# Performance work log

Hardware: AMD Instinct MI355X
Metric: run time of the kernel (lower is better)

The kernel has to match this reference:

```python
import jax, jax.numpy as jnp
import numpy as np

H = W = 256
SIZE, STRIDE = 16, 8
NUMS = (H - SIZE) // STRIDE + 1   # 31
L = NUMS * NUMS                   # 961
S2 = SIZE * SIZE                  # 256
EPS = 1e-5
B, C = 2, 64


def _rel_pos_index(h, w):
    ch, cw = np.arange(h), np.arange(w)
    coords = np.stack(np.meshgrid(ch, cw, indexing='ij'))      # [2,h,w]
    cf = coords.reshape(2, -1)                                  # [2,h*w]
    rel = (cf[:, :, None] - cf[:, None, :]).transpose(1, 2, 0)  # [L,L,2]
    rel = rel.copy()
    rel[:, :, 0] += h - 1
    rel[:, :, 1] += w - 1
    rel[:, :, 0] *= 2 * w - 1
    return jnp.asarray(rel.sum(-1))                             # [L,L] int

REL_IDX = _rel_pos_index(NUMS, NUMS)


def unfold(x):
    # torch.nn.Unfold(kernel=SIZE, stride=STRIDE): [B,C,H,W] -> [B, C*S2, L]
    b, c = x.shape[:2]
    p = jax.lax.conv_general_dilated_patches(x, (SIZE, SIZE), (STRIDE, STRIDE), 'VALID')
    return p.reshape(b, c * S2, L)


def fold(cols, c):
    # torch.nn.Fold: [B, c*S2, L] -> [B, c, H, W] via overlap scatter-add
    b = cols.shape[0]
    p = cols.reshape(b, c, SIZE, SIZE, NUMS, NUMS)          # [b,c,kh,kw,oh,ow]
    idx = jnp.arange(SIZE)[:, None] + STRIDE * jnp.arange(NUMS)[None, :]  # [SIZE,NUMS]
    hfull = idx[:, None, :, None]   # [kh,1,oh,1]
    wfull = idx[None, :, None, :]   # [1,kw,1,ow]
    out = jnp.zeros((b, c, H, W), cols.dtype)
    return out.at[:, :, hfull, wfull].add(p)


def fg_mean_std(region, mask):
    # masked spatial mean / std; region = x*mask already
    s = region.sum((2, 3))                                   # [B,C]
    num = mask.sum((2, 3))                                   # [B,1]
    mu = (s / (num + EPS))[:, :, None, None]                 # [B,C,1,1]
    # region + (1-mask)*mu - mu == region - mask*mu
    var = (((region - mask * mu) ** 2).sum((2, 3)) / (num + EPS))[:, :, None, None]
    return mu, jnp.sqrt(var + EPS)


def setup_inputs() -> dict:
    key = jax.random.key(0)
    ks = jax.random.split(key, 12)
    x = jax.random.normal(ks[0], (B, C, H, W), jnp.float32)
    mask = (jax.random.uniform(ks[1], (B, 1, H, W)) > 0.5).astype(jnp.float32)
    def v(k, scale=0.02, off=0.0):
        return off + scale * jax.random.normal(k, (C,), jnp.float32)
    return {
        'x': x, 'mask': mask,
        'fg_gamma': v(ks[2]), 'fg_beta': v(ks[3]),
        'bg_gamma': v(ks[4]), 'bg_beta': v(ks[5]),
        'q_gamma': v(ks[6], off=1.0), 'q_beta': v(ks[7]),
        'k_gamma': v(ks[8], off=1.0), 'k_beta': v(ks[9]),
        'bias_table': 0.02 * jax.random.normal(ks[10], ((2 * NUMS - 1) ** 2,), jnp.float32),
    }


def reference(x, mask, fg_gamma, fg_beta, bg_gamma, bg_beta,
              q_gamma, q_beta, k_gamma, k_beta, bias_table):
    om = 1.0 - mask
    mean_b, std_b = fg_mean_std(x * om, om)
    normalized = (x - mean_b) / std_b * om
    norm_bg = (x * (1 + bg_gamma[None, :, None, None]) + bg_beta[None, :, None, None]) * om
    mean_f, std_f = fg_mean_std(x * mask, mask)
    norm_fg = (x - mean_f) / std_f * mask

    # unfold to [B,C,L,S2] (torch: view(B,C,S2,L).permute(0,1,3,2))
    pb = unfold(x * om).reshape(B, C, S2, L).transpose(0, 1, 3, 2)
    npf = unfold(norm_fg).reshape(B, C, S2, L).transpose(0, 1, 3, 2)
    npb = unfold(normalized).reshape(B, C, S2, L).transpose(0, 1, 3, 2)
    pm = unfold(mask).reshape(B, 1, S2, L).transpose(0, 1, 3, 2)
    count_cols = unfold(jnp.ones((1, 1, H, W), x.dtype))     # [1,S2,L]

    # per-patch masked stats (note: 'std' is actually variance, as in original)
    num = (1.0 - pm).sum(3)                                   # [B,1,L]
    mu1 = pb.sum(3) / (num + EPS)                             # [B,C,L]
    var1 = (((pb - (1.0 - pm) * mu1[..., None]) ** 2).sum(3)) / (num + EPS)
    mu4 = npb.sum(3) / (num + EPS)
    numm = pm.sum(3)
    mu3 = npf.sum(3) / (numm + EPS)

    q = mu3 * q_gamma[None, :, None] + q_beta[None, :, None]
    k = mu4 * k_gamma[None, :, None] + k_beta[None, :, None]

    bias = bias_table[REL_IDX.reshape(-1)].reshape(L, L)
    Smat = jax.nn.softmax(jnp.einsum('bcl,bcm->blm', q, k) + bias[None], axis=-1)
    patch_back = jnp.einsum('blm,bcm->bcl', Smat, mu1)[..., None]   # [B,C,L,1]
    patch_std = jnp.einsum('blm,bcm->bcl', Smat, var1)[..., None]

    npf2 = npf * patch_std + patch_back                        # [B,C,L,S2]
    cols = npf2.transpose(0, 1, 3, 2).reshape(B, C * S2, L)
    cnt = fold(count_cols, 1)                                  # [1,1,H,W]
    nf = fold(cols, C) / cnt
    nf = (nf * (1 + fg_gamma[None, :, None, None]) + fg_beta[None, :, None, None]) * mask
    return nf + norm_bg
```

## Files before the change

### kernel.cpp

```cpp
#include <hip/hip_runtime.h>
#include <hip/hip_fp16.h>
#include <cmath>

constexpr int H = 256, W = 256;
constexpr int NUMS = 31;
constexpr int L = NUMS * NUMS;
constexpr int B = 2, C = 64;
constexpr float EPS = 1e-5f;

constexpr int NL = 8;
constexpr int NGROUP = 121;
constexpr int LPAD = 968;
constexpr int MPAD = 976;
constexpr int M2 = 488;

typedef __fp16 h2 __attribute__((ext_vector_type(2)));

__device__ inline h2 pk2(float a, float b) {
#if __has_builtin(__builtin_amdgcn_cvt_pkrtz)
    return __builtin_amdgcn_cvt_pkrtz(a, b);
#else
    h2 r; r.x = (__fp16)a; r.y = (__fp16)b; return r;
#endif
}
__device__ inline float h2f(h2 v) { return __builtin_bit_cast(float, v); }
__device__ inline h2 f2h(float v) { return __builtin_bit_cast(h2, v); }

#if __has_builtin(__builtin_amdgcn_fdot2)
#define FDOT2(a, b, c) __builtin_amdgcn_fdot2((a), (b), (c), false)
#else
#define FDOT2(a, b, c) ((c) + (float)(a).x * (float)(b).x + (float)(a).y * (float)(b).y)
#endif

__global__ __launch_bounds__(256) void cellsum_kernel(
    const float* __restrict__ x, const float* __restrict__ mask,
    float4* __restrict__ cellsA, float* __restrict__ cellsM)
{
    int cr = blockIdx.x, c = blockIdx.y, b = blockIdx.z;
    int t = threadIdx.x, r = t >> 5, cc = t & 31;
    const float* xp = x + (((size_t)(b * C + c) * H) + cr * 8 + r) * W + cc * 8;
    const float* mp = mask + (((size_t)b * H) + cr * 8 + r) * W + cc * 8;

    float s0 = 0.f, s1 = 0.f, s2 = 0.f, s3 = 0.f, nf = 0.f;
#pragma unroll
    for (int q = 0; q < 2; ++q) {
        float4 xv = ((const float4*)xp)[q];
        float4 mv = ((const float4*)mp)[q];
        float xs[4] = {xv.x, xv.y, xv.z, xv.w};
        float ms[4] = {mv.x, mv.y, mv.z, mv.w};
#pragma unroll
        for (int j = 0; j < 4; ++j) {
            float xx = xs[j], m = ms[j], om = 1.f - m;
            s0 += xx * om; s1 += xx * xx * om;
            s2 += xx;      s3 += xx * xx;
            nf += m;
        }
    }
    s0 += __shfl_xor(s0, 32); s1 += __shfl_xor(s1, 32);
    s2 += __shfl_xor(s2, 32); s3 += __shfl_xor(s3, 32);
    nf += __shfl_xor(nf, 32);

    __shared__ float red[4][32][5];
    int wv = t >> 6;
    if ((t & 63) < 32) {
        red[wv][cc][0] = s0; red[wv][cc][1] = s1; red[wv][cc][2] = s2;
        red[wv][cc][3] = s3; red[wv][cc][4] = nf;
    }
    __syncthreads();
    if (t < 32) {
        float a0 = red[0][t][0] + red[1][t][0] + red[2][t][0] + red[3][t][0];
        float a1 = red[0][t][1] + red[1][t][1] + red[2][t][1] + red[3][t][1];
        float a2 = red[0][t][2] + red[1][t][2] + red[2][t][2] + red[3][t][2];
        float a3 = red[0][t][3] + red[1][t][3] + red[2][t][3] + red[3][t][3];
        float an = red[0][t][4] + red[1][t][4] + red[2][t][4] + red[3][t][4];
        int cell = cr * 32 + t;
        cellsA[((size_t)b * 1024 + cell) * C + c] = make_float4(a0, a1, a2, a3);
        if (c == 0) cellsM[(size_t)b * 1024 + cell] = an;
    }
}

__global__ __launch_bounds__(256) void stats_kernel(
    const float4* __restrict__ cellsA, const float* __restrict__ cellsM,
    float* __restrict__ stats)
{
    int c = blockIdx.x, b = blockIdx.y, t = threadIdx.x;
    float s0 = 0.f, s1 = 0.f, s2 = 0.f, s3 = 0.f, nf = 0.f;
    for (int e = t; e < 1024; e += 256) {
        float4 v = cellsA[((size_t)b * 1024 + e) * C + c];
        s0 += v.x; s1 += v.y; s2 += v.z; s3 += v.w;
        nf += cellsM[(size_t)b * 1024 + e];
    }
#pragma unroll
    for (int off = 32; off; off >>= 1) {
        s0 += __shfl_xor(s0, off); s1 += __shfl_xor(s1, off);
        s2 += __shfl_xor(s2, off); s3 += __shfl_xor(s3, off);
        nf += __shfl_xor(nf, off);
    }
    __shared__ float red[4][5];
    if ((t & 63) == 0) {
        red[t >> 6][0] = s0; red[t >> 6][1] = s1; red[t >> 6][2] = s2;
        red[t >> 6][3] = s3; red[t >> 6][4] = nf;
    }
    __syncthreads();
    if (t == 0) {
        float a0 = red[0][0] + red[1][0] + red[2][0] + red[3][0];
        float a1 = red[0][1] + red[1][1] + red[2][1] + red[3][1];
        float a2 = red[0][2] + red[1][2] + red[2][2] + red[3][2];
        float a3 = red[0][3] + red[1][3] + red[2][3] + red[3][3];
        float an = red[0][4] + red[1][4] + red[2][4] + red[3][4];
        float numbg = (float)(H * W) - an;
        float mu_b = a0 / (numbg + EPS);
        float var_b = (a1 - 2.f * mu_b * a0 + mu_b * mu_b * numbg) / (numbg + EPS);
        float sxfg = a2 - a0, sxxfg = a3 - a1;
        float mu_f = sxfg / (an + EPS);
        float var_f = (sxxfg - 2.f * mu_f * sxfg + mu_f * mu_f * an) / (an + EPS);
        float* st = stats + ((size_t)b * C + c) * 4;
        st[0] = mu_b; st[1] = 1.f / sqrtf(var_b + EPS);
        st[2] = mu_f; st[3] = 1.f / sqrtf(var_f + EPS);
    }
}

__global__ __launch_bounds__(256) void patchfinal_kernel(
    const float4* __restrict__ cellsA, const float* __restrict__ cellsM,
    const float* __restrict__ stats,
    const float* __restrict__ qg, const float* __restrict__ qb,
    const float* __restrict__ kg, const float* __restrict__ kb,
    float* __restrict__ qTT, float* __restrict__ kTT, float2* __restrict__ mvh)
{
    int lq = blockIdx.x, b = blockIdx.y;
    int t = threadIdx.x, ls = t >> 6, c = t & 63;
    int l = lq * 4 + ls;

    float mu1 = 0.f, var1 = 0.f, qv = 0.f, kv = 0.f;
    if (l < L) {
        int lh = l / 31, lw = l % 31;
        int e00 = lh * 32 + lw;
        size_t base = (size_t)b * 1024;
        float4 s00 = cellsA[(base + e00) * C + c];
        float4 s01 = cellsA[(base + e00 + 1) * C + c];
        float4 s10 = cellsA[(base + e00 + 32) * C + c];
        float4 s11 = cellsA[(base + e00 + 33) * C + c];
        float sxbg = s00.x + s01.x + s10.x + s11.x;
        float sxxbg = s00.y + s01.y + s10.y + s11.y;
        float sxall = s00.z + s01.z + s10.z + s11.z;
        float nfg = cellsM[base + e00] + cellsM[base + e00 + 1]
                  + cellsM[base + e00 + 32] + cellsM[base + e00 + 33];
        float numbg = 256.f - nfg;
        float rb = 1.f / (numbg + EPS), rf = 1.f / (nfg + EPS);
        const float* st = stats + ((size_t)b * C + c) * 4;
        float mu_b = st[0], isb = st[1], mu_f = st[2], isf = st[3];
        mu1 = sxbg * rb;
        var1 = (sxxbg - 2.f * mu1 * sxbg + mu1 * mu1 * numbg) * rb;
        float mu4 = (sxbg - mu_b * numbg) * isb * rb;
        float sxfg = sxall - sxbg;
        float mu3 = (sxfg - mu_f * nfg) * isf * rf;
        qv = mu3 * qg[c] + qb[c];
        kv = mu4 * kg[c] + kb[c];
    }
    qTT[((size_t)(b * C + c)) * LPAD + l] = qv;
    kTT[((size_t)(b * C + c)) * MPAD + l] = kv;

    __shared__ float smu[4][64], svar[4][64];
    smu[ls][c] = mu1; svar[ls][c] = var1;
    __syncthreads();
    if (t < 128) {
        int p = t >> 6, cc = t & 63;
        h2 mp_ = pk2(smu[2 * p][cc], smu[2 * p + 1][cc]);
        h2 vp_ = pk2(svar[2 * p][cc], svar[2 * p + 1][cc]);
        mvh[((size_t)b * M2 + lq * 2 + p) * C + cc] = make_float2(h2f(mp_), h2f(vp_));
    }
}

__global__ __launch_bounds__(512) void attn_kernel(
    const float* __restrict__ qTT, const float* __restrict__ kTT,
    const float2* __restrict__ mvh, const float* __restrict__ bias_table,
    float* __restrict__ pbTc, float* __restrict__ psTc)
{
    __shared__ float4 wlds[M2][2];
    __shared__ float parts[8][NL][65][2];
    __shared__ float rsp[8][NL];

    int g = blockIdx.x, b = blockIdx.y;
    int t = threadIdx.x, l0 = g * NL;
    int m0 = t, m1 = t + 512;
    int m1c = m1 < MPAD ? m1 : MPAD - 1;

    int lhs[NL], lws[NL];
#pragma unroll
    for (int li = 0; li < NL; ++li) {
        int l = l0 + li; if (l > L - 1) l = L - 1;
        lhs[li] = l / 31; lws[li] = l % 31;
    }

    float dot0[NL] = {0, 0, 0, 0, 0, 0, 0, 0};
    float dot1[NL] = {0, 0, 0, 0, 0, 0, 0, 0};
    const float* kbase = kTT + (size_t)b * C * MPAD;
    const float* qbase = qTT + (size_t)b * C * LPAD + l0;
#pragma unroll 4
    for (int c = 0; c < C; ++c) {
        float k0 = kbase[(size_t)c * MPAD + m0];
        float k1 = kbase[(size_t)c * MPAD + m1c];
        const float* qp = qbase + (size_t)c * LPAD;
#pragma unroll
        for (int li = 0; li < NL; ++li) {
            float q = qp[li];
            dot0[li] = fmaf(q, k0, dot0[li]);
            dot1[li] = fmaf(q, k1, dot1[li]);
        }
    }

    float e0[NL], e1[NL];
    float psum[NL] = {0, 0, 0, 0, 0, 0, 0, 0};
    {
        int mh = m0 / 31, mw = m0 - mh * 31;
#pragma unroll
        for (int li = 0; li < NL; ++li) {
            float bias = bias_table[(lhs[li] - mh + 30) * 61 + (lws[li] - mw + 30)];
            e0[li] = __expf(dot0[li] + bias);
            psum[li] += e0[li];
        }
    }
    if (m1 < L) {
        int mh = m1 / 31, mw = m1 - mh * 31;
#pragma unroll
        for (int li = 0; li < NL; ++li) {
            float bias = bias_table[(lhs[li] - mh + 30) * 61 + (lws[li] - mw + 30)];
            e1[li] = __expf(dot1[li] + bias);
            psum[li] += e1[li];
        }
    } else {
#pragma unroll
        for (int li = 0; li < NL; ++li) e1[li] = 0.f;
    }

    {
        float n0[NL], n1[NL];
#pragma unroll
        for (int li = 0; li < NL; ++li) {
            n0[li] = __shfl_down(e0[li], 1);
            n1[li] = __shfl_down(e1[li], 1);
        }
        if (!(t & 1)) {
            wlds[m0 >> 1][0] = make_float4(h2f(pk2(e0[0], n0[0])), h2f(pk2(e0[1], n0[1])),
                                           h2f(pk2(e0[2], n0[2])), h2f(pk2(e0[3], n0[3])));
            wlds[m0 >> 1][1] = make_float4(h2f(pk2(e0[4], n0[4])), h2f(pk2(e0[5], n0[5])),
                                           h2f(pk2(e0[6], n0[6])), h2f(pk2(e0[7], n0[7])));
            if (m1 < MPAD) {
                wlds[m1 >> 1][0] = make_float4(h2f(pk2(e1[0], n1[0])), h2f(pk2(e1[1], n1[1])),
                                               h2f(pk2(e1[2], n1[2])), h2f(pk2(e1[3], n1[3])));
                wlds[m1 >> 1][1] = make_float4(h2f(pk2(e1[4], n1[4])), h2f(pk2(e1[5], n1[5])),
                                               h2f(pk2(e1[6], n1[6])), h2f(pk2(e1[7], n1[7])));
            }
        }
    }
#pragma unroll
    for (int li = 0; li < NL; ++li) {
        float v = psum[li];
#pragma unroll
        for (int off = 32; off; off >>= 1) v += __shfl_xor(v, off);
        if ((t & 63) == 0) rsp[t >> 6][li] = v;
    }
    __syncthreads();

    int wv = t >> 6, c = t & 63;
    float accb[NL] = {0, 0, 0, 0, 0, 0, 0, 0};
    float accs[NL] = {0, 0, 0, 0, 0, 0, 0, 0};
    const float2* vbase = mvh + (size_t)b * M2 * C + c;
    int mstart = wv * 61;
#pragma unroll 2
    for (int i = 0; i < 61; ++i) {
        int m2 = mstart + i;
        float4 wa = wlds[m2][0];
        float4 wb = wlds[m2][1];
        float2 v = vbase[(size_t)m2 * C];
        h2 vb = f2h(v.x), vs = f2h(v.y);
        accb[0] = FDOT2(f2h(wa.x), vb, accb[0]); accs[0] = FDOT2(f2h(wa.x), vs, accs[0]);
        accb[1] = FDOT2(f2h(wa.y), vb, accb[1]); accs[1] = FDOT2(f2h(wa.y), vs, accs[1]);
        accb[2] = FDOT2(f2h(wa.z), vb, accb[2]); accs[2] = FDOT2(f2h(wa.z), vs, accs[2]);
        accb[3] = FDOT2(f2h(wa.w), vb, accb[3]); accs[3] = FDOT2(f2h(wa.w), vs, accs[3]);
        accb[4] = FDOT2(f2h(wb.x), vb, accb[4]); accs[4] = FDOT2(f2h(wb.x), vs, accs[4]);
        accb[5] = FDOT2(f2h(wb.y), vb, accb[5]); accs[5] = FDOT2(f2h(wb.y), vs, accs[5]);
        accb[6] = FDOT2(f2h(wb.z), vb, accb[6]); accs[6] = FDOT2(f2h(wb.z), vs, accs[6]);
        accb[7] = FDOT2(f2h(wb.w), vb, accb[7]); accs[7] = FDOT2(f2h(wb.w), vs, accs[7]);
    }
#pragma unroll
    for (int li = 0; li < NL; ++li) {
        parts[wv][li][c][0] = accb[li];
        parts[wv][li][c][1] = accs[li];
    }
    __syncthreads();

    {
        int li = t & 7, co = t >> 3;
        float sb = 0.f, ss = 0.f, rs = 0.f;
#pragma unroll
        for (int w = 0; w < 8; ++w) {
            sb += parts[w][li][co][0];
            ss += parts[w][li][co][1];
            rs += rsp[w][li];
        }
        if (l0 + li < L) {
            float inv = 1.f / rs;
            size_t o = ((size_t)(b * C + co)) * LPAD + l0 + li;
            pbTc[o] = sb * inv;
            psTc[o] = ss * inv;
        }
    }
}

__global__ __launch_bounds__(256) void out_kernel(
    const float* __restrict__ x, const float* __restrict__ mask,
    const float* __restrict__ stats,
    const float* __restrict__ pbTc, const float* __restrict__ psTc,
    const float* __restrict__ fgg, const float* __restrict__ fgb,
    const float* __restrict__ bgg, const float* __restrict__ bgb,
    float* __restrict__ out)
{
    int idx = blockIdx.x * 256 + threadIdx.x;
    int w4 = idx & (W / 4 - 1);
    int rest = idx >> 6;
    int h = rest & (H - 1);
    int bc = rest >> 8;
    int c = bc & (C - 1);
    int b = bc >> 6;
    int w = w4 * 4;

    size_t pix = ((size_t)bc * H + h) * W + w;
    float4 xv = *(const float4*)&x[pix];
    float4 mv = *(const float4*)&mask[((size_t)b * H + h) * W + w];

    const float* st = stats + (size_t)bc * 4;
    float mu_f = st[2], isf = st[3];

    int hq = h >> 3, wq = w >> 3;
    int ph0 = hq > 0 ? hq - 1 : 0;
    int ph1 = hq < NUMS ? hq : NUMS - 1;
    int pw0 = wq > 0 ? wq - 1 : 0;
    int pw1 = wq < NUMS ? wq : NUMS - 1;

    const float* pbc = pbTc + (size_t)bc * LPAD;
    const float* psc = psTc + (size_t)bc * LPAD;

    float sstd = 0.f, sback = 0.f;
    for (int ph = ph0; ph <= ph1; ++ph) {
        int base = ph * 31;
        for (int pw = pw0; pw <= pw1; ++pw) {
            sstd += psc[base + pw];
            sback += pbc[base + pw];
        }
    }
    float rcnt = 1.f / (float)((ph1 - ph0 + 1) * (pw1 - pw0 + 1));
    float ga = 1.f + fgg[c], be = fgb[c];
    float gb_ = 1.f + bgg[c], bb = bgb[c];

    float xs[4] = {xv.x, xv.y, xv.z, xv.w};
    float ms_[4] = {mv.x, mv.y, mv.z, mv.w};
    float4 res;
    float* rp = &res.x;
#pragma unroll
    for (int j = 0; j < 4; ++j) {
        float nfg_px = (xs[j] - mu_f) * isf * ms_[j];
        float nf = (nfg_px * sstd + sback) * rcnt;
        rp[j] = (nf * ga + be) * ms_[j] + (xs[j] * gb_ + bb) * (1.f - ms_[j]);
    }
    *(float4*)&out[pix] = res;
}

extern "C" void kernel_launch(void* const* d_in, const int* in_sizes, int n_in,
                              void* d_out, int out_size, void* d_ws, size_t ws_size,
                              hipStream_t stream)
{
    const float* x    = (const float*)d_in[0];
    const float* mask = (const float*)d_in[1];
    const float* fgg  = (const float*)d_in[2];
    const float* fgb  = (const float*)d_in[3];
    const float* bgg  = (const float*)d_in[4];
    const float* bgb  = (const float*)d_in[5];
    const float* qg   = (const float*)d_in[6];
    const float* qb   = (const float*)d_in[7];
    const float* kg   = (const float*)d_in[8];
    const float* kb   = (const float*)d_in[9];
    const float* bt   = (const float*)d_in[10];
    float* out = (float*)d_out;

    float* ws = (float*)d_ws;
    float4* cellsA = (float4*)ws;
    float* cellsM  = ws + (size_t)B * 1024 * C * 4;
    float* stats   = cellsM + (size_t)B * 1024;
    float* qTT     = stats + (size_t)B * C * 4;
    float* kTT     = qTT + (size_t)B * C * LPAD;
    float2* mvh    = (float2*)(kTT + (size_t)B * C * MPAD);
    float* pbTc    = (float*)mvh + (size_t)B * M2 * C * 2;
    float* psTc    = pbTc + (size_t)B * C * LPAD;

    cellsum_kernel<<<dim3(32, C, B), 256, 0, stream>>>(x, mask, cellsA, cellsM);
    stats_kernel<<<dim3(C, B), 256, 0, stream>>>(cellsA, cellsM, stats);
    patchfinal_kernel<<<dim3(241, B), 256, 0, stream>>>(
        cellsA, cellsM, stats, qg, qb, kg, kb, qTT, kTT, mvh);
    attn_kernel<<<dim3(NGROUP, B), 512, 0, stream>>>(qTT, kTT, mvh, bt, pbTc, psTc);
    out_kernel<<<(B * C * H * W / 4 + 255) / 256, 256, 0, stream>>>(
        x, mask, stats, pbTc, psTc, fgg, fgb, bgg, bgb, out);
}
```

Before: 69.32 us.

## Halve attention rows per block and precompute fold averages in a separate kernel

```diff
diff --git a/kernel.cpp b/kernel.cpp
--- a/kernel.cpp
+++ b/kernel.cpp
@@ -8,8 +8,8 @@
 constexpr int B = 2, C = 64;
 constexpr float EPS = 1e-5f;
 
-constexpr int NL = 8;
-constexpr int NGROUP = 121;
+constexpr int NL = 4;
+constexpr int NGROUP = 241;
 constexpr int LPAD = 968;
 constexpr int MPAD = 976;
 constexpr int M2 = 488;
@@ -171,19 +171,17 @@
     }
 }
 
-__global__ __launch_bounds__(512) void attn_kernel(
+__global__ __launch_bounds__(256) void attn_kernel(
     const float* __restrict__ qTT, const float* __restrict__ kTT,
     const float2* __restrict__ mvh, const float* __restrict__ bias_table,
     float* __restrict__ pbTc, float* __restrict__ psTc)
 {
-    __shared__ float4 wlds[M2][2];
-    __shared__ float parts[8][NL][65][2];
-    __shared__ float rsp[8][NL];
+    __shared__ float4 wlds[M2];
+    __shared__ float parts[4][NL][65][2];
+    __shared__ float rsp[4][NL];
 
     int g = blockIdx.x, b = blockIdx.y;
     int t = threadIdx.x, l0 = g * NL;
-    int m0 = t, m1 = t + 512;
-    int m1c = m1 < MPAD ? m1 : MPAD - 1;
 
     int lhs[NL], lws[NL];
 #pragma unroll
@@ -192,65 +190,62 @@
         lhs[li] = l / 31; lws[li] = l % 31;
     }
 
-    float dot0[NL] = {0, 0, 0, 0, 0, 0, 0, 0};
-    float dot1[NL] = {0, 0, 0, 0, 0, 0, 0, 0};
+    int mm[4] = {t, t + 256, t + 512, t + 768};
+    int m3c = mm[3] < MPAD ? mm[3] : MPAD - 1;
+
+    float dot[4][NL];
+#pragma unroll
+    for (int j = 0; j < 4; ++j)
+#pragma unroll
+        for (int li = 0; li < NL; ++li) dot[j][li] = 0.f;
+
     const float* kbase = kTT + (size_t)b * C * MPAD;
     const float* qbase = qTT + (size_t)b * C * LPAD + l0;
-#pragma unroll 4
+#pragma unroll 2
     for (int c = 0; c < C; ++c) {
-        float k0 = kbase[(size_t)c * MPAD + m0];
-        float k1 = kbase[(size_t)c * MPAD + m1c];
+        float k0 = kbase[(size_t)c * MPAD + mm[0]];
+        float k1 = kbase[(size_t)c * MPAD + mm[1]];
+        float k2 = kbase[(size_t)c * MPAD + mm[2]];
+        float k3 = kbase[(size_t)c * MPAD + m3c];
         const float* qp = qbase + (size_t)c * LPAD;
 #pragma unroll
         for (int li = 0; li < NL; ++li) {
             float q = qp[li];
-            dot0[li] = fmaf(q, k0, dot0[li]);
-            dot1[li] = fmaf(q, k1, dot1[li]);
-        }
-    }
-
-    float e0[NL], e1[NL];
-    float psum[NL] = {0, 0, 0, 0, 0, 0, 0, 0};
-    {
-        int mh = m0 / 31, mw = m0 - mh * 31;
-#pragma unroll
-        for (int li = 0; li < NL; ++li) {
-            float bias = bias_table[(lhs[li] - mh + 30) * 61 + (lws[li] - mw + 30)];
-            e0[li] = __expf(dot0[li] + bias);
-            psum[li] += e0[li];
-        }
-    }
-    if (m1 < L) {
-        int mh = m1 / 31, mw = m1 - mh * 31;
-#pragma unroll
-        for (int li = 0; li < NL; ++li) {
-            float bias = bias_table[(lhs[li] - mh + 30) * 61 + (lws[li] - mw + 30)];
-            e1[li] = __expf(dot1[li] + bias);
-            psum[li] += e1[li];
-        }
-    } else {
-#pragma unroll
-        for (int li = 0; li < NL; ++li) e1[li] = 0.f;
-    }
-
-    {
-        float n0[NL], n1[NL];
-#pragma unroll
-        for (int li = 0; li < NL; ++li) {
-            n0[li] = __shfl_down(e0[li], 1);
-            n1[li] = __shfl_down(e1[li], 1);
-        }
-        if (!(t & 1)) {
-            wlds[m0 >> 1][0] = make_float4(h2f(pk2(e0[0], n0[0])), h2f(pk2(e0[1], n0[1])),
-                                           h2f(pk2(e0[2], n0[2])), h2f(pk2(e0[3], n0[3])));
-            wlds[m0 >> 1][1] = make_float4(h2f(pk2(e0[4], n0[4])), h2f(pk2(e0[5], n0[5])),
-                                           h2f(pk2(e0[6], n0[6])), h2f(pk2(e0[7], n0[7])));
-            if (m1 < MPAD) {
-                wlds[m1 >> 1][0] = make_float4(h2f(pk2(e1[0], n1[0])), h2f(pk2(e1[1], n1[1])),
-                                               h2f(pk2(e1[2], n1[2])), h2f(pk2(e1[3], n1[3])));
-                wlds[m1 >> 1][1] = make_float4(h2f(pk2(e1[4], n1[4])), h2f(pk2(e1[5], n1[5])),
-                                               h2f(pk2(e1[6], n1[6])), h2f(pk2(e1[7], n1[7])));
+            dot[0][li] = fmaf(q, k0, dot[0][li]);
+            dot[1][li] = fmaf(q, k1, dot[1][li]);
+            dot[2][li] = fmaf(q, k2, dot[2][li]);
+            dot[3][li] = fmaf(q, k3, dot[3][li]);
+        }
+    }
+
+    float e[4][NL];
+    float psum[NL] = {0.f, 0.f, 0.f, 0.f};
+#pragma unroll
+    for (int j = 0; j < 4; ++j) {
+        int m = mm[j];
+        if (m < L) {
+            int mh = m / 31, mw = m - (m / 31) * 31;
+#pragma unroll
+            for (int li = 0; li < NL; ++li) {
+                float bias = bias_table[(lhs[li] - mh + 30) * 61 + (lws[li] - mw + 30)];
+                e[j][li] = __expf(dot[j][li] + bias);
+                psum[li] += e[j][li];
             }
+        } else {
+#pragma unroll
+            for (int li = 0; li < NL; ++li) e[j][li] = 0.f;
+        }
+    }
+
+#pragma unroll
+    for (int j = 0; j < 4; ++j) {
+        float n0 = __shfl_down(e[j][0], 1);
+        float n1 = __shfl_down(e[j][1], 1);
+        float n2 = __shfl_down(e[j][2], 1);
+        float n3 = __shfl_down(e[j][3], 1);
+        if (!(t & 1) && mm[j] < MPAD) {
+            wlds[mm[j] >> 1] = make_float4(h2f(pk2(e[j][0], n0)), h2f(pk2(e[j][1], n1)),
+                                           h2f(pk2(e[j][2], n2)), h2f(pk2(e[j][3], n3)));
         }
     }
 #pragma unroll
@@ -262,39 +257,55 @@
     }
     __syncthreads();
 
-    int wv = t >> 6, c = t & 63;
-    float accb[NL] = {0, 0, 0, 0, 0, 0, 0, 0};
-    float accs[NL] = {0, 0, 0, 0, 0, 0, 0, 0};
-    const float2* vbase = mvh + (size_t)b * M2 * C + c;
-    int mstart = wv * 61;
-#pragma unroll 2
-    for (int i = 0; i < 61; ++i) {
-        int m2 = mstart + i;
-        float4 wa = wlds[m2][0];
-        float4 wb = wlds[m2][1];
-        float2 v = vbase[(size_t)m2 * C];
-        h2 vb = f2h(v.x), vs = f2h(v.y);
-        accb[0] = FDOT2(f2h(wa.x), vb, accb[0]); accs[0] = FDOT2(f2h(wa.x), vs, accs[0]);
-        accb[1] = FDOT2(f2h(wa.y), vb, accb[1]); accs[1] = FDOT2(f2h(wa.y), vs, accs[1]);
-        accb[2] = FDOT2(f2h(wa.z), vb, accb[2]); accs[2] = FDOT2(f2h(wa.z), vs, accs[2]);
-        accb[3] = FDOT2(f2h(wa.w), vb, accb[3]); accs[3] = FDOT2(f2h(wa.w), vs, accs[3]);
-        accb[4] = FDOT2(f2h(wb.x), vb, accb[4]); accs[4] = FDOT2(f2h(wb.x), vs, accs[4]);
-        accb[5] = FDOT2(f2h(wb.y), vb, accb[5]); accs[5] = FDOT2(f2h(wb.y), vs, accs[5]);
-        accb[6] = FDOT2(f2h(wb.z), vb, accb[6]); accs[6] = FDOT2(f2h(wb.z), vs, accs[6]);
-        accb[7] = FDOT2(f2h(wb.w), vb, accb[7]); accs[7] = FDOT2(f2h(wb.w), vs, accs[7]);
-    }
+    int wv = t >> 6, lane = t & 63;
+    int mg = lane >> 4, ci = lane & 15;
+    float accb[NL][4], accs[NL][4];
+#pragma unroll
+    for (int li = 0; li < NL; ++li)
+#pragma unroll
+        for (int cs = 0; cs < 4; ++cs) { accb[li][cs] = 0.f; accs[li][cs] = 0.f; }
+
+    const float2* vbase = mvh + (size_t)b * M2 * C;
+    int moff = (wv << 2) + mg;
+    for (int i = 0; i < 31; ++i) {
+        int m2 = i * 16 + moff;
+        if (m2 < M2) {
+            float4 w4 = wlds[m2];
+            h2 w0 = f2h(w4.x), w1 = f2h(w4.y), w2 = f2h(w4.z), w3 = f2h(w4.w);
+            const float2* vp = vbase + (size_t)m2 * C + ci;
+#pragma unroll
+            for (int cs = 0; cs < 4; ++cs) {
+                float2 v = vp[cs * 16];
+                h2 vb = f2h(v.x), vs = f2h(v.y);
+                accb[0][cs] = FDOT2(w0, vb, accb[0][cs]); accs[0][cs] = FDOT2(w0, vs, accs[0][cs]);
+                accb[1][cs] = FDOT2(w1, vb, accb[1][cs]); accs[1][cs] = FDOT2(w1, vs, accs[1][cs]);
+                accb[2][cs] = FDOT2(w2, vb, accb[2][cs]); accs[2][cs] = FDOT2(w2, vs, accs[2][cs]);
+                accb[3][cs] = FDOT2(w3, vb, accb[3][cs]); accs[3][cs] = FDOT2(w3, vs, accs[3][cs]);
+            }
+        }
+    }
+#pragma unroll
+    for (int li = 0; li < NL; ++li)
+#pragma unroll
+        for (int cs = 0; cs < 4; ++cs) {
+            accb[li][cs] += __shfl_xor(accb[li][cs], 16);
+            accb[li][cs] += __shfl_xor(accb[li][cs], 32);
+            accs[li][cs] += __shfl_xor(accs[li][cs], 16);
+            accs[li][cs] += __shfl_xor(accs[li][cs], 32);
+        }
+    int cout = (mg << 4) + ci;
 #pragma unroll
     for (int li = 0; li < NL; ++li) {
-        parts[wv][li][c][0] = accb[li];
-        parts[wv][li][c][1] = accs[li];
+        parts[wv][li][cout][0] = accb[li][mg];
+        parts[wv][li][cout][1] = accs[li][mg];
     }
     __syncthreads();
 
     {
-        int li = t & 7, co = t >> 3;
+        int li = t & 3, co = t >> 2;
         float sb = 0.f, ss = 0.f, rs = 0.f;
 #pragma unroll
-        for (int w = 0; w < 8; ++w) {
+        for (int w = 0; w < 4; ++w) {
             sb += parts[w][li][co][0];
             ss += parts[w][li][co][1];
             rs += rsp[w][li];
@@ -308,10 +319,34 @@
     }
 }
 
+__global__ __launch_bounds__(256) void fold_kernel(
+    const float* __restrict__ pbTc, const float* __restrict__ psTc,
+    float2* __restrict__ fold)
+{
+    int idx = blockIdx.x * 256 + threadIdx.x;
+    int cell = idx & 1023, bc = idx >> 10;
+    int hq = cell >> 5, wq = cell & 31;
+    int ph0 = hq > 0 ? hq - 1 : 0;
+    int ph1 = hq < NUMS ? hq : NUMS - 1;
+    int pw0 = wq > 0 ? wq - 1 : 0;
+    int pw1 = wq < NUMS ? wq : NUMS - 1;
+    const float* pbc = pbTc + (size_t)bc * LPAD;
+    const float* psc = psTc + (size_t)bc * LPAD;
+    float sb = 0.f, ss = 0.f;
+    for (int ph = ph0; ph <= ph1; ++ph) {
+        int base = ph * 31;
+        for (int pw = pw0; pw <= pw1; ++pw) {
+            sb += pbc[base + pw];
+            ss += psc[base + pw];
+        }
+    }
+    float rc = 1.f / (float)((ph1 - ph0 + 1) * (pw1 - pw0 + 1));
+    fold[idx] = make_float2(sb * rc, ss * rc);
+}
+
 __global__ __launch_bounds__(256) void out_kernel(
     const float* __restrict__ x, const float* __restrict__ mask,
-    const float* __restrict__ stats,
-    const float* __restrict__ pbTc, const float* __restrict__ psTc,
+    const float* __restrict__ stats, const float2* __restrict__ fold,
     const float* __restrict__ fgg, const float* __restrict__ fgb,
     const float* __restrict__ bgg, const float* __restrict__ bgb,
     float* __restrict__ out)
@@ -332,24 +367,10 @@
     const float* st = stats + (size_t)bc * 4;
     float mu_f = st[2], isf = st[3];
 
-    int hq = h >> 3, wq = w >> 3;
-    int ph0 = hq > 0 ? hq - 1 : 0;
-    int ph1 = hq < NUMS ? hq : NUMS - 1;
-    int pw0 = wq > 0 ? wq - 1 : 0;
-    int pw1 = wq < NUMS ? wq : NUMS - 1;
-
-    const float* pbc = pbTc + (size_t)bc * LPAD;
-    const float* psc = psTc + (size_t)bc * LPAD;
-
-    float sstd = 0.f, sback = 0.f;
-    for (int ph = ph0; ph <= ph1; ++ph) {
-        int base = ph * 31;
-        for (int pw = pw0; pw <= pw1; ++pw) {
-            sstd += psc[base + pw];
-            sback += pbc[base + pw];
-        }
-    }
-    float rcnt = 1.f / (float)((ph1 - ph0 + 1) * (pw1 - pw0 + 1));
+    int cell = ((h >> 3) << 5) + (w >> 3);
+    float2 f = fold[(size_t)bc * 1024 + cell];
+    float fback = f.x, fstd = f.y;
+
     float ga = 1.f + fgg[c], be = fgb[c];
     float gb_ = 1.f + bgg[c], bb = bgb[c];
 
@@ -360,7 +381,7 @@
 #pragma unroll
     for (int j = 0; j < 4; ++j) {
         float nfg_px = (xs[j] - mu_f) * isf * ms_[j];
-        float nf = (nfg_px * sstd + sback) * rcnt;
+        float nf = nfg_px * fstd + fback;
         rp[j] = (nf * ga + be) * ms_[j] + (xs[j] * gb_ + bb) * (1.f - ms_[j]);
     }
     *(float4*)&out[pix] = res;
@@ -392,12 +413,14 @@
     float2* mvh    = (float2*)(kTT + (size_t)B * C * MPAD);
     float* pbTc    = (float*)mvh + (size_t)B * M2 * C * 2;
     float* psTc    = pbTc + (size_t)B * C * LPAD;
+    float2* fold   = (float2*)(psTc + (size_t)B * C * LPAD);
 
     cellsum_kernel<<<dim3(32, C, B), 256, 0, stream>>>(x, mask, cellsA, cellsM);
     stats_kernel<<<dim3(C, B), 256, 0, stream>>>(cellsA, cellsM, stats);
     patchfinal_kernel<<<dim3(241, B), 256, 0, stream>>>(
         cellsA, cellsM, stats, qg, qb, kg, kb, qTT, kTT, mvh);
-    attn_kernel<<<dim3(NGROUP, B), 512, 0, stream>>>(qTT, kTT, mvh, bt, pbTc, psTc);
+    attn_kernel<<<dim3(NGROUP, B), 256, 0, stream>>>(qTT, kTT, mvh, bt, pbTc, psTc);
+    fold_kernel<<<(B * C * 1024) / 256, 256, 0, stream>>>(pbTc, psTc, fold);
     out_kernel<<<(B * C * H * W / 4 + 255) / 256, 256, 0, stream>>>(
-        x, mask, stats, pbTc, psTc, fgg, fgb, bgg, bgb, out);
-}
+        x, mask, stats, fold, fgg, fgb, bgg, bgb, out);
+}
```

After: 63.47 us. 8.4% less time.
